# Kernel optimization log

Hardware: AMD Instinct MI355X
Metric: run time of the kernel (lower is better)

The kernel has to match this reference:

```python
import jax, jax.numpy as jnp
import numpy as np
from jax import lax

DIM = 384
NUM_HEADS = 6
STRIDE_Q = 1
STRIDE_KV = 2
BN_EPS = 1e-5
SCALE = DIM ** (-0.5)  # CvT scales by dim_out, not head_dim


def setup_inputs() -> dict:
    key = jax.random.key(0)
    ks = jax.random.split(key, 8)
    B, H, W, C = 32, 28, 28, DIM
    T = 1 + H * W
    x = jax.random.normal(ks[0], (B, T, C), dtype=jnp.float32)
    conv_w = jax.random.normal(ks[1], (3, C, 1, 3, 3), dtype=jnp.float32) * 0.1
    bn_gamma = jnp.ones((3, C), dtype=jnp.float32)
    bn_beta = jnp.zeros((3, C), dtype=jnp.float32)
    bn_mean = jnp.zeros((3, C), dtype=jnp.float32)
    bn_var = jnp.ones((3, C), dtype=jnp.float32)
    w_q = jax.random.normal(ks[2], (C, C), dtype=jnp.float32) * 0.02
    w_k = jax.random.normal(ks[3], (C, C), dtype=jnp.float32) * 0.02
    w_v = jax.random.normal(ks[4], (C, C), dtype=jnp.float32) * 0.02
    w_proj = jax.random.normal(ks[5], (C, C), dtype=jnp.float32) * 0.02
    b_proj = jnp.zeros((C,), dtype=jnp.float32)
    return {"x": x, "conv_w": conv_w, "bn_gamma": bn_gamma, "bn_beta": bn_beta,
            "bn_mean": bn_mean, "bn_var": bn_var, "w_q": w_q, "w_k": w_k,
            "w_v": w_v, "w_proj": w_proj, "b_proj": b_proj, "h": H, "w": W}


def _dw_conv_bn(x_sp, cw, gamma, beta, mean, var, stride):
    # x_sp: [B, C, H, W]; cw: [C, 1, 3, 3] depthwise (groups=C); inference BN
    C = x_sp.shape[1]
    y = lax.conv_general_dilated(
        x_sp, cw, window_strides=(stride, stride), padding=((1, 1), (1, 1)),
        feature_group_count=C, dimension_numbers=("NCHW", "OIHW", "NCHW"))
    inv = gamma * lax.rsqrt(var + BN_EPS)
    y = y * inv[None, :, None, None] + (beta - mean * inv)[None, :, None, None]
    B, Cc, Hc, Wc = y.shape
    return y.reshape(B, Cc, Hc * Wc).transpose(0, 2, 1)  # b (h w) c


def reference(x, conv_w, bn_gamma, bn_beta, bn_mean, bn_var,
              w_q, w_k, w_v, w_proj, b_proj, h, w):
    B, T, C = x.shape
    nh, hd = NUM_HEADS, C // NUM_HEADS
    cls_tok, x_tok = x[:, :1], x[:, 1:]
    x_sp = x_tok.reshape(B, h, w, C).transpose(0, 3, 1, 2)  # b c h w

    q = _dw_conv_bn(x_sp, conv_w[0], bn_gamma[0], bn_beta[0], bn_mean[0], bn_var[0], STRIDE_Q)
    k = _dw_conv_bn(x_sp, conv_w[1], bn_gamma[1], bn_beta[1], bn_mean[1], bn_var[1], STRIDE_KV)
    v = _dw_conv_bn(x_sp, conv_w[2], bn_gamma[2], bn_beta[2], bn_mean[2], bn_var[2], STRIDE_KV)

    q = jnp.concatenate([cls_tok, q], axis=1)
    k = jnp.concatenate([cls_tok, k], axis=1)
    v = jnp.concatenate([cls_tok, v], axis=1)

    def split_heads(t, wm):  # linear proj then b t (h d) -> b h t d
        t = t @ wm.T
        Bt, Tt, _ = t.shape
        return t.reshape(Bt, Tt, nh, hd).transpose(0, 2, 1, 3)

    q = split_heads(q, w_q)
    k = split_heads(k, w_k)
    v = split_heads(v, w_v)

    attn = jax.nn.softmax(jnp.einsum("bhld,bhtd->bhlt", q, k) * SCALE, axis=-1)
    out = jnp.einsum("bhlt,bhtd->bhld", attn, v)
    out = out.transpose(0, 2, 1, 3).reshape(B, -1, C)  # b t (h d)
    return out @ w_proj.T + b_proj
```

## Files before the change

kernel.cpp:

```cpp
#include <hip/hip_runtime.h>
#include <math.h>

#define B_SZ   32
#define C_DIM  384
#define H_IN   28
#define W_IN   28
#define TQ     785
#define TKV    197
#define NH     6
#define HD     64
#define SCALE_F 0.05103103630798287f
#define SCALE_L2E (0.05103103630798287f * 1.4426950408889634f)
#define BN_EPS_F 1e-5f

#define QROWS    25120
#define KVROWS   6304
#define QROWS_P  25344
#define KVROWS_P 6528
#define WELEM    147456
#define VT_LD    208

#define QT256    99
#define KVT256   25

typedef _Float16 f16;
typedef f16  f16x8 __attribute__((ext_vector_type(8)));
typedef f16  f16x4 __attribute__((ext_vector_type(4)));
typedef float f32x4 __attribute__((ext_vector_type(4)));

__device__ __forceinline__ void split16(float v, f16& h, f16& l) {
    h = (f16)v;
    l = (f16)(v - (float)h);
}

__device__ __forceinline__ void cp16(void* lds, const void* g) {
    __builtin_amdgcn_global_load_lds(
        (const __attribute__((address_space(1))) unsigned int*)g,
        (__attribute__((address_space(3))) unsigned int*)lds, 16, 0, 0);
}

__device__ __forceinline__ bool swz(int id, int yMax, int& y, int& n0) {
    int g = id / 24, w = id - g * 24;
    y = g * 8 + (w & 7);
    n0 = (w >> 3) * 128;
    return y < yMax;
}

__global__ __launch_bounds__(256) void prep_kernel(
    const float* __restrict__ wq, const float* __restrict__ wk,
    const float* __restrict__ wv, const float* __restrict__ wp,
    const float* __restrict__ conv_w,
    const float* __restrict__ gamma, const float* __restrict__ beta,
    const float* __restrict__ mean, const float* __restrict__ var,
    f16* __restrict__ Wh, f16* __restrict__ Wl,
    float* __restrict__ wAll)
{
    int idx = blockIdx.x * 256 + threadIdx.x;
    if (idx < 4 * WELEM) {
        int which = idx / WELEM, rem = idx - which * WELEM;
        const float* s = (which == 0) ? wq : (which == 1) ? wk : (which == 2) ? wv : wp;
        float v = s[rem];
        if (which == 0) v *= SCALE_L2E;
        f16 h, l;
        split16(v, h, l);
        Wh[idx] = h; Wl[idx] = l;
    } else if (idx < 4 * WELEM + 3 * C_DIM) {
        int k = idx - 4 * WELEM;
        int cv = k / C_DIM, c = k - cv * C_DIM;
        float inv = gamma[k] * rsqrtf(var[k] + BN_EPS_F);
#pragma unroll
        for (int t = 0; t < 9; ++t)
            wAll[cv * 3840 + t * C_DIM + c] = conv_w[(size_t)cv * C_DIM * 9 + c * 9 + t] * inv;
        wAll[cv * 3840 + 9 * C_DIM + c] = beta[k] - mean[k] * inv;
    }
}

__global__ __launch_bounds__(256) void fused_conv_kernel(
    const float* __restrict__ x,
    const float* __restrict__ wAll,
    f16* __restrict__ qh, f16* __restrict__ ql,
    f16* __restrict__ kh, f16* __restrict__ kl,
    f16* __restrict__ vh, f16* __restrict__ vl)
{
    __shared__ float sW[3 * 3840];
    int tid = threadIdx.x;
    int oi = blockIdx.x, b = blockIdx.y;

    if (oi == H_IN) {
        if (tid < 96) {
            int c = tid * 4;
            float4 v = *(const float4*)&x[(size_t)b * TQ * C_DIM + c];
            float a[4] = {v.x, v.y, v.z, v.w};
            f16x4 hv, lv;
#pragma unroll
            for (int u = 0; u < 4; ++u) { f16 h, l; split16(a[u], h, l); hv[u] = h; lv[u] = l; }
            size_t oq = (size_t)b * TQ * C_DIM + c;
            size_t okv = (size_t)b * TKV * C_DIM + c;
            *(f16x4*)&qh[oq] = hv;  *(f16x4*)&ql[oq] = lv;
            *(f16x4*)&kh[okv] = hv; *(f16x4*)&kl[okv] = lv;
            *(f16x4*)&vh[okv] = hv; *(f16x4*)&vl[okv] = lv;
        }
        return;
    }

#pragma unroll
    for (int i = 0; i < 12; ++i) {
        int idx = tid + 256 * i;
        if (idx < 2880) cp16(&sW[idx * 4], &wAll[idx * 4]);
    }
    __syncthreads();

    const size_t xb = (size_t)b * TQ * C_DIM + C_DIM;
    bool oi_even = (oi & 1) == 0;

    for (int it = 0; it < 11; ++it) {
        int idx = tid + 256 * it;
        if (idx >= 28 * 96) break;
        int oj = idx / 96, cg = idx - oj * 96;
        int c = cg * 4;

        float4 xv[9];
#pragma unroll
        for (int di = 0; di < 3; ++di) {
            int ii = oi + di - 1;
            bool rok = (ii >= 0) && (ii < H_IN);
#pragma unroll
            for (int dj = 0; dj < 3; ++dj) {
                int jj = oj + dj - 1;
                bool ok = rok && (jj >= 0) && (jj < W_IN);
                xv[di * 3 + dj] = ok ? *(const float4*)&x[xb + ((size_t)ii * W_IN + jj) * C_DIM + c]
                                     : make_float4(0.f, 0.f, 0.f, 0.f);
            }
        }

        {
            float4 acc = *(const float4*)&sW[0 * 3840 + 9 * C_DIM + c];
#pragma unroll
            for (int t = 0; t < 9; ++t) {
                float4 w4 = *(const float4*)&sW[0 * 3840 + t * C_DIM + c];
                acc.x += w4.x * xv[t].x; acc.y += w4.y * xv[t].y;
                acc.z += w4.z * xv[t].z; acc.w += w4.w * xv[t].w;
            }
            f16x4 hv, lv;
            float a[4] = {acc.x, acc.y, acc.z, acc.w};
#pragma unroll
            for (int u = 0; u < 4; ++u) { f16 h, l; split16(a[u], h, l); hv[u] = h; lv[u] = l; }
            size_t off = ((size_t)b * TQ + 1 + oi * W_IN + oj) * C_DIM + c;
            *(f16x4*)&qh[off] = hv;
            *(f16x4*)&ql[off] = lv;
        }

        if (oi_even && ((oj & 1) == 0)) {
            int p = (oi >> 1) * 14 + (oj >> 1);
            size_t off = ((size_t)b * TKV + 1 + p) * C_DIM + c;
#pragma unroll
            for (int cv = 1; cv <= 2; ++cv) {
                float4 acc = *(const float4*)&sW[cv * 3840 + 9 * C_DIM + c];
#pragma unroll
                for (int t = 0; t < 9; ++t) {
                    float4 w4 = *(const float4*)&sW[cv * 3840 + t * C_DIM + c];
                    acc.x += w4.x * xv[t].x; acc.y += w4.y * xv[t].y;
                    acc.z += w4.z * xv[t].z; acc.w += w4.w * xv[t].w;
                }
                f16x4 hv, lv;
                float a[4] = {acc.x, acc.y, acc.z, acc.w};
#pragma unroll
                for (int u = 0; u < 4; ++u) { f16 h, l; split16(a[u], h, l); hv[u] = h; lv[u] = l; }
                if (cv == 1) { *(f16x4*)&kh[off] = hv; *(f16x4*)&kl[off] = lv; }
                else         { *(f16x4*)&vh[off] = hv; *(f16x4*)&vl[off] = lv; }
            }
        }
    }
}

__device__ __forceinline__ void gemm_body(
    const f16* __restrict__ Ah, const f16* __restrict__ Al,
    const f16* __restrict__ Wh, const f16* __restrict__ Wl,
    const float* __restrict__ bias,
    float* __restrict__ Cf, f16* __restrict__ Coh, f16* __restrict__ Col,
    int M, int mode, int m0, int n0)
{
    __shared__ f16 lds[3 * 24576];

    const int t = threadIdx.x;
    const int wv = t >> 6, lane = t & 63;
    const int wr = (wv >> 1) * 64;
    const int wc = (wv & 1) * 64;
    const int lrow = lane & 15, quad = lane >> 4;
    const int qsw = quad ^ ((lrow >> 1) & 3);

    const int sr = t >> 2;
    const int g  = (t & 3) ^ ((t >> 3) & 3);

    const f16* gA0h = Ah + (size_t)(m0 + sr) * 384 + g * 8;
    const f16* gA1h = gA0h + 128 * 384;
    const f16* gA0l = Al + (size_t)(m0 + sr) * 384 + g * 8;
    const f16* gA1l = gA0l + 128 * 384;
    const f16* gBh  = Wh + (size_t)(n0 + sr) * 384 + g * 8;
    const f16* gBl  = Wl + (size_t)(n0 + sr) * 384 + g * 8;

#define STAGE(buf, kk) do {                                   \
        f16* d = lds + (buf) * 24576 + t * 8;                 \
        const int ko = (kk) * 32;                             \
        cp16(d,         gA0h + ko);                           \
        cp16(d + 4096,  gA1h + ko);                           \
        cp16(d + 8192,  gA0l + ko);                           \
        cp16(d + 12288, gA1l + ko);                           \
        cp16(d + 16384, gBh + ko);                            \
        cp16(d + 20480, gBl + ko);                            \
    } while (0)

    f32x4 acc[4][4];
#pragma unroll
    for (int i = 0; i < 4; ++i)
#pragma unroll
        for (int j = 0; j < 4; ++j)
            acc[i][j] = (f32x4){0.f, 0.f, 0.f, 0.f};

    STAGE(0, 0);
    STAGE(1, 1);

#pragma unroll
    for (int kk = 0; kk < 12; ++kk) {
        if (kk == 11) asm volatile("s_waitcnt vmcnt(0)" ::: "memory");
        else          asm volatile("s_waitcnt vmcnt(6)" ::: "memory");
        __builtin_amdgcn_s_barrier();
        __builtin_amdgcn_sched_barrier(0);

        if (kk < 10) {
            STAGE((kk + 2) % 3, kk + 2);
            __builtin_amdgcn_sched_barrier(0);
        }

        const f16* bp = lds + (kk % 3) * 24576;
        f16x8 ah[4], al[4], bh[4], bl[4];
#pragma unroll
        for (int i = 0; i < 4; ++i) {
            int ro = (wr + i * 16 + lrow) * 32 + qsw * 8;
            ah[i] = *(const f16x8*)&bp[ro];
            al[i] = *(const f16x8*)&bp[8192 + ro];
        }
#pragma unroll
        for (int j = 0; j < 4; ++j) {
            int ro = (wc + j * 16 + lrow) * 32 + qsw * 8;
            bh[j] = *(const f16x8*)&bp[16384 + ro];
            bl[j] = *(const f16x8*)&bp[20480 + ro];
        }
        asm volatile("s_waitcnt lgkmcnt(0)" ::: "memory");
        __builtin_amdgcn_sched_barrier(0);

        __builtin_amdgcn_s_setprio(1);
#pragma unroll
        for (int i = 0; i < 4; ++i)
#pragma unroll
            for (int j = 0; j < 4; ++j) {
                acc[i][j] = __builtin_amdgcn_mfma_f32_16x16x32_f16(ah[i], bh[j], acc[i][j], 0, 0, 0);
                acc[i][j] = __builtin_amdgcn_mfma_f32_16x16x32_f16(ah[i], bl[j], acc[i][j], 0, 0, 0);
                acc[i][j] = __builtin_amdgcn_mfma_f32_16x16x32_f16(al[i], bh[j], acc[i][j], 0, 0, 0);
            }
        __builtin_amdgcn_s_setprio(0);
    }
#undef STAGE

#pragma unroll
    for (int i = 0; i < 4; ++i) {
        int grow0 = m0 + wr + i * 16 + quad * 4;
#pragma unroll
        for (int j = 0; j < 4; ++j) {
            int gcol = n0 + wc + j * 16 + lrow;
            float bb = (bias && mode == 0) ? bias[gcol] : 0.f;
#pragma unroll
            for (int r = 0; r < 4; ++r) {
                int grow = grow0 + r;
                if (grow >= M) continue;
                float v = acc[i][j][r] + bb;
                if (mode == 0) {
                    Cf[(size_t)grow * 384 + gcol] = v;
                } else if (mode == 1) {
                    f16 h, l;
                    split16(v, h, l);
                    Coh[(size_t)grow * 384 + gcol] = h;
                    Col[(size_t)grow * 384 + gcol] = l;
                } else {
                    int bb2 = grow / TKV;
                    int key = grow - bb2 * TKV;
                    size_t off = (size_t)bb2 * 384 * VT_LD + (size_t)gcol * VT_LD + key;
                    Coh[off] = (f16)v;
                }
            }
        }
    }
}

__device__ __forceinline__ void gemm_body_s(
    const f16* __restrict__ Ah,
    const f16* __restrict__ Wh, const f16* __restrict__ Wl,
    const float* __restrict__ bias, float* __restrict__ Cf,
    int M, int m0, int n0)
{
    __shared__ f16 lds[3 * 16384];

    const int t = threadIdx.x;
    const int wv = t >> 6, lane = t & 63;
    const int wr = (wv >> 1) * 64;
    const int wc = (wv & 1) * 64;
    const int lrow = lane & 15, quad = lane >> 4;
    const int qsw = quad ^ ((lrow >> 1) & 3);

    const int sr = t >> 2;
    const int g  = (t & 3) ^ ((t >> 3) & 3);

    const f16* gA0 = Ah + (size_t)(m0 + sr) * 384 + g * 8;
    const f16* gA1 = gA0 + 128 * 384;
    const f16* gBh = Wh + (size_t)(n0 + sr) * 384 + g * 8;
    const f16* gBl = Wl + (size_t)(n0 + sr) * 384 + g * 8;

#define STAGE_S(buf, kk) do {                                 \
        f16* d = lds + (buf) * 16384 + t * 8;                 \
        const int ko = (kk) * 32;                             \
        cp16(d,         gA0 + ko);                            \
        cp16(d + 4096,  gA1 + ko);                            \
        cp16(d + 8192,  gBh + ko);                            \
        cp16(d + 12288, gBl + ko);                            \
    } while (0)

    f32x4 acc[4][4];
#pragma unroll
    for (int i = 0; i < 4; ++i)
#pragma unroll
        for (int j = 0; j < 4; ++j)
            acc[i][j] = (f32x4){0.f, 0.f, 0.f, 0.f};

    STAGE_S(0, 0);
    STAGE_S(1, 1);

#pragma unroll
    for (int kk = 0; kk < 12; ++kk) {
        if (kk == 11) asm volatile("s_waitcnt vmcnt(0)" ::: "memory");
        else          asm volatile("s_waitcnt vmcnt(4)" ::: "memory");
        __builtin_amdgcn_s_barrier();
        __builtin_amdgcn_sched_barrier(0);

        if (kk < 10) {
            STAGE_S((kk + 2) % 3, kk + 2);
            __builtin_amdgcn_sched_barrier(0);
        }

        const f16* bp = lds + (kk % 3) * 16384;
        f16x8 ah[4], bh[4], bl[4];
#pragma unroll
        for (int i = 0; i < 4; ++i) {
            int ro = (wr + i * 16 + lrow) * 32 + qsw * 8;
            ah[i] = *(const f16x8*)&bp[ro];
        }
#pragma unroll
        for (int j = 0; j < 4; ++j) {
            int ro = (wc + j * 16 + lrow) * 32 + qsw * 8;
            bh[j] = *(const f16x8*)&bp[8192 + ro];
            bl[j] = *(const f16x8*)&bp[12288 + ro];
        }
        asm volatile("s_waitcnt lgkmcnt(0)" ::: "memory");
        __builtin_amdgcn_sched_barrier(0);

        __builtin_amdgcn_s_setprio(1);
#pragma unroll
        for (int i = 0; i < 4; ++i)
#pragma unroll
            for (int j = 0; j < 4; ++j) {
                acc[i][j] = __builtin_amdgcn_mfma_f32_16x16x32_f16(ah[i], bh[j], acc[i][j], 0, 0, 0);
                acc[i][j] = __builtin_amdgcn_mfma_f32_16x16x32_f16(ah[i], bl[j], acc[i][j], 0, 0, 0);
            }
        __builtin_amdgcn_s_setprio(0);
    }
#undef STAGE_S

#pragma unroll
    for (int i = 0; i < 4; ++i) {
        int grow0 = m0 + wr + i * 16 + quad * 4;
#pragma unroll
        for (int j = 0; j < 4; ++j) {
            int gcol = n0 + wc + j * 16 + lrow;
            float bb = bias[gcol];
#pragma unroll
            for (int r = 0; r < 4; ++r) {
                int grow = grow0 + r;
                if (grow >= M) continue;
                Cf[(size_t)grow * 384 + gcol] = acc[i][j][r] + bb;
            }
        }
    }
}

__global__ __launch_bounds__(512, 2) void qkv_proj_kernel(
    const f16* __restrict__ qh, const f16* __restrict__ ql,
    const f16* __restrict__ kh, const f16* __restrict__ kl,
    const f16* __restrict__ vh, const f16* __restrict__ vl,
    const f16* __restrict__ Wh, const f16* __restrict__ Wl,
    f16* __restrict__ Qph, f16* __restrict__ Qpl,
    f16* __restrict__ Kph, f16* __restrict__ Kpl,
    f16* __restrict__ VTh,
    int yMax)
{
    int y, n0;
    if (!swz(blockIdx.x, yMax, y, n0)) return;
    if (y < QT256)
        gemm_body(qh, ql, Wh, Wl, nullptr, nullptr, Qph, Qpl, QROWS, 1, y * 256, n0);
    else if (y < QT256 + KVT256)
        gemm_body(kh, kl, Wh + WELEM, Wl + WELEM, nullptr, nullptr, Kph, Kpl,
                  KVROWS, 1, (y - QT256) * 256, n0);
    else
        gemm_body(vh, vl, Wh + 2 * WELEM, Wl + 2 * WELEM, nullptr, nullptr, VTh, nullptr,
                  KVROWS, 2, (y - QT256 - KVT256) * 256, n0);
}

__global__ __launch_bounds__(512, 2) void v_proj_kernel(
    const f16* __restrict__ vh, const f16* __restrict__ vl,
    const f16* __restrict__ Wh, const f16* __restrict__ Wl,
    f16* __restrict__ VTh)
{
    int y, n0;
    if (!swz(blockIdx.x, KVT256, y, n0)) return;
    gemm_body(vh, vl, Wh, Wl, nullptr, nullptr, VTh, nullptr, KVROWS, 2, y * 256, n0);
}

__global__ __launch_bounds__(512, 2) void out_proj_kernel(
    const f16* __restrict__ Ah,
    const f16* __restrict__ Wh, const f16* __restrict__ Wl,
    const float* __restrict__ bias, float* __restrict__ Cf)
{
    int y, n0;
    if (!swz(blockIdx.x, QT256, y, n0)) return;
    gemm_body_s(Ah, Wh, Wl, bias, Cf, QROWS, y * 256, n0);
}

__global__ __launch_bounds__(256) void attn_mfma6(
    const f16* __restrict__ Qh, const f16* __restrict__ Ql,
    const f16* __restrict__ Kh, const f16* __restrict__ Kl,
    const f16* __restrict__ VTh,
    f16* __restrict__ Oh)
{
    __shared__ f16 sQh[2][64][32];
    __shared__ f16 sQl[2][64][32];
    __shared__ f16 sKh[2][64][32];
    __shared__ f16 sKl[2][64][32];
    __shared__ float sPs[64][68];

    int t = threadIdx.x;
    int wv = t >> 6, lane = t & 63;
    int c = lane & 15, quad = lane >> 4;
    int wq0 = wv * 16;
    int h = blockIdx.y, b = blockIdx.z;
    int q0 = blockIdx.x * 64;

    const size_t qbase  = (size_t)b * TQ * C_DIM + h * HD;
    const size_t kbase  = (size_t)b * TKV * C_DIM + h * HD;
    const size_t vtbase = (size_t)b * 384 * VT_LD + (size_t)h * HD * VT_LD;

#pragma unroll
    for (int i = 0; i < 2; ++i) {
        int idx = t + 256 * i;
        int ks = idx >> 8, row = (idx >> 2) & 63, sg = (idx & 3) * 8;
        cp16(&sQh[ks][row][sg], &Qh[qbase + (size_t)(q0 + row) * C_DIM + ks * 32 + sg]);
        cp16(&sQl[ks][row][sg], &Ql[qbase + (size_t)(q0 + row) * C_DIM + ks * 32 + sg]);
    }

    f32x4 s[4][4];
#pragma unroll
    for (int kt = 0; kt < 4; ++kt)
#pragma unroll
        for (int j = 0; j < 4; ++j)
            s[kt][j] = (f32x4){0.f, 0.f, 0.f, 0.f};

#pragma unroll
    for (int kt = 0; kt < 4; ++kt) {
        if (kt) __syncthreads();
#pragma unroll
        for (int i = 0; i < 2; ++i) {
            int idx = t + 256 * i;
            int ks = idx >> 8, row = (idx >> 2) & 63, sg = (idx & 3) * 8;
            cp16(&sKh[ks][row][sg], &Kh[kbase + (size_t)(kt * 64 + row) * C_DIM + ks * 32 + sg]);
            cp16(&sKl[ks][row][sg], &Kl[kbase + (size_t)(kt * 64 + row) * C_DIM + ks * 32 + sg]);
        }
        __syncthreads();

#pragma unroll
        for (int ks = 0; ks < 2; ++ks) {
            f16x8 qh8 = *(const f16x8*)&sQh[ks][wq0 + c][quad * 8];
            f16x8 ql8 = *(const f16x8*)&sQl[ks][wq0 + c][quad * 8];
#pragma unroll
            for (int j = 0; j < 4; ++j) {
                f16x8 kh8 = *(const f16x8*)&sKh[ks][j * 16 + c][quad * 8];
                f16x8 kl8 = *(const f16x8*)&sKl[ks][j * 16 + c][quad * 8];
                s[kt][j] = __builtin_amdgcn_mfma_f32_16x16x32_f16(qh8, kh8, s[kt][j], 0, 0, 0);
                s[kt][j] = __builtin_amdgcn_mfma_f32_16x16x32_f16(qh8, kl8, s[kt][j], 0, 0, 0);
                s[kt][j] = __builtin_amdgcn_mfma_f32_16x16x32_f16(ql8, kh8, s[kt][j], 0, 0, 0);
            }
        }
    }

    __syncthreads();

#pragma unroll
    for (int i = 0; i < 2; ++i) {
        int idx = t + 256 * i;
        int ks = idx >> 8, row = (idx >> 2) & 63, sg = (idx & 3) * 8;
        cp16(&sKh[ks][row][sg], &VTh[vtbase + (size_t)row * VT_LD + ks * 32 + sg]);
        cp16(&sKl[ks][row][sg], &VTh[vtbase + (size_t)row * VT_LD + 64 + ks * 32 + sg]);
    }

#pragma unroll
    for (int r = 0; r < 4; ++r) {
        s[3][0][r] = (c < 5) ? s[3][0][r] : -1e30f;
        s[3][1][r] = -1e30f;
        s[3][2][r] = -1e30f;
        s[3][3][r] = -1e30f;
    }

    float inv_r[4];
#pragma unroll
    for (int r = 0; r < 4; ++r) {
        float mx = -1e30f;
#pragma unroll
        for (int kt = 0; kt < 4; ++kt)
#pragma unroll
            for (int j = 0; j < 4; ++j)
                mx = fmaxf(mx, s[kt][j][r]);
        mx = fmaxf(mx, __shfl_xor(mx, 1));
        mx = fmaxf(mx, __shfl_xor(mx, 2));
        mx = fmaxf(mx, __shfl_xor(mx, 4));
        mx = fmaxf(mx, __shfl_xor(mx, 8));
        float sum = 0.f;
#pragma unroll
        for (int kt = 0; kt < 4; ++kt)
#pragma unroll
            for (int j = 0; j < 4; ++j) {
                float pv = exp2f(s[kt][j][r] - mx);
                s[kt][j][r] = pv;
                sum += pv;
            }
        sum += __shfl_xor(sum, 1);
        sum += __shfl_xor(sum, 2);
        sum += __shfl_xor(sum, 4);
        sum += __shfl_xor(sum, 8);
        inv_r[r] = 1.f / sum;
    }

    f32x4 o[4];
#pragma unroll
    for (int j = 0; j < 4; ++j) o[j] = (f32x4){0.f, 0.f, 0.f, 0.f};

#define SPS_WRITE(VT) do {                                           \
        _Pragma("unroll") for (int r = 0; r < 4; ++r)                \
            _Pragma("unroll") for (int j = 0; j < 4; ++j)            \
                sPs[wq0 + quad * 4 + r][j * 16 + c] = s[VT][j][r];   \
    } while (0)

#define VT_ISSUE2(DST, VT) do {                                                \
        _Pragma("unroll") for (int i = 0; i < 2; ++i) {                        \
            int idx = t + 256 * i;                                             \
            int ks = idx >> 8, row = (idx >> 2) & 63, sg = (idx & 3) * 8;      \
            cp16(&DST[ks][row][sg],                                            \
                 &VTh[vtbase + (size_t)row * VT_LD + (VT) * 64 + ks * 32 + sg]); \
        } } while (0)

#define PV_TILE_S(BUF) do {                                                    \
        _Pragma("unroll") for (int ks = 0; ks < 2; ++ks) {                     \
            float4 p0 = *(const float4*)&sPs[wq0 + c][ks * 32 + quad * 8];     \
            float4 p1 = *(const float4*)&sPs[wq0 + c][ks * 32 + quad * 8 + 4]; \
            float pf[8] = {p0.x, p0.y, p0.z, p0.w, p1.x, p1.y, p1.z, p1.w};    \
            f16x8 p8;                                                          \
            _Pragma("unroll") for (int ii = 0; ii < 8; ++ii) p8[ii] = (f16)pf[ii]; \
            _Pragma("unroll") for (int j = 0; j < 4; ++j) {                    \
                f16x8 vv8 = *(const f16x8*)&BUF[ks][j * 16 + c][quad * 8];     \
                o[j] = __builtin_amdgcn_mfma_f32_16x16x32_f16(p8, vv8, o[j], 0, 0, 0); \
            } } } while (0)

    __syncthreads();
    SPS_WRITE(0);
    PV_TILE_S(sKh);
    __syncthreads();
    VT_ISSUE2(sKh, 2);
    SPS_WRITE(1);
    PV_TILE_S(sKl);
    __syncthreads();
    VT_ISSUE2(sKl, 3);
    SPS_WRITE(2);
    PV_TILE_S(sKh);
    __syncthreads();
    SPS_WRITE(3);
    PV_TILE_S(sKl);

#pragma unroll
    for (int r = 0; r < 4; ++r) {
        int gq = q0 + wq0 + quad * 4 + r;
        if (gq >= TQ) continue;
        float inv = inv_r[r];
#pragma unroll
        for (int j = 0; j < 4; ++j) {
            size_t off = (size_t)(b * TQ + gq) * C_DIM + h * HD + j * 16 + c;
            Oh[off] = (f16)(o[j][r] * inv);
        }
    }
#undef SPS_WRITE
#undef VT_ISSUE2
#undef PV_TILE_S
}

extern "C" void kernel_launch(void* const* d_in, const int* in_sizes, int n_in,
                              void* d_out, int out_size, void* d_ws, size_t ws_size,
                              hipStream_t stream) {
    const float* x       = (const float*)d_in[0];
    const float* conv_w  = (const float*)d_in[1];
    const float* bn_g    = (const float*)d_in[2];
    const float* bn_b    = (const float*)d_in[3];
    const float* bn_m    = (const float*)d_in[4];
    const float* bn_v    = (const float*)d_in[5];
    const float* w_q     = (const float*)d_in[6];
    const float* w_k     = (const float*)d_in[7];
    const float* w_v     = (const float*)d_in[8];
    const float* w_proj  = (const float*)d_in[9];
    const float* b_proj  = (const float*)d_in[10];
    float* out = (float*)d_out;

    const size_t QSZ   = (size_t)QROWS_P * 384 * sizeof(f16);
    const size_t KVSZ  = (size_t)KVROWS_P * 384 * sizeof(f16);
    const size_t WSZ   = 4 * (size_t)WELEM * sizeof(f16);
    const size_t VTSZ  = (size_t)B_SZ * 384 * VT_LD * sizeof(f16);
    const size_t WALLS = 3 * 3840 * sizeof(float);

    char* p = (char*)d_ws;
    f16* qh  = (f16*)p; p += QSZ;
    f16* ql  = (f16*)p; p += QSZ;
    f16* vh  = (f16*)p; p += KVSZ;
    f16* vl  = (f16*)p; p += KVSZ;
    f16* kh  = (f16*)p; p += KVSZ;
    f16* kl  = (f16*)p; p += KVSZ;
    f16* Wh  = (f16*)p; p += WSZ;
    f16* Wl  = (f16*)p; p += WSZ;
    f16* Qph = (f16*)p; p += QSZ;
    f16* Qpl = (f16*)p; p += QSZ;
    f16* Kph = (f16*)p; p += KVSZ;
    f16* Kpl = (f16*)p; p += KVSZ;
    float* wAll = (float*)p; p += WALLS;

    size_t used = (size_t)(p - (char*)d_ws);
    bool sepVT = (ws_size >= used + VTSZ);
    f16* VTh = sepVT ? (f16*)p : kh;
    f16* oh = qh;

    {
        int total = 4 * WELEM + 3 * C_DIM;
        prep_kernel<<<(total + 255) / 256, 256, 0, stream>>>(
            w_q, w_k, w_v, w_proj, conv_w, bn_g, bn_b, bn_m, bn_v, Wh, Wl, wAll);
    }

    {
        dim3 gc(H_IN + 1, B_SZ);
        fused_conv_kernel<<<gc, 256, 0, stream>>>(x, wAll, qh, ql, kh, kl, vh, vl);
    }

    if (sepVT) {
        int yMax = QT256 + 2 * KVT256;
        int nb = ((yMax + 7) / 8) * 24;
        qkv_proj_kernel<<<nb, 512, 0, stream>>>(qh, ql, kh, kl, vh, vl, Wh, Wl,
                                                Qph, Qpl, Kph, Kpl, VTh, yMax);
    } else {
        int yMax = QT256 + KVT256;
        int nb = ((yMax + 7) / 8) * 24;
        qkv_proj_kernel<<<nb, 512, 0, stream>>>(qh, ql, kh, kl, vh, vl, Wh, Wl,
                                                Qph, Qpl, Kph, Kpl, VTh, yMax);
        int nbv = ((KVT256 + 7) / 8) * 24;
        v_proj_kernel<<<nbv, 512, 0, stream>>>(vh, vl, Wh + 2 * WELEM, Wl + 2 * WELEM,
                                               VTh);
    }

    {
        dim3 ga((TQ + 63) / 64, NH, B_SZ);
        attn_mfma6<<<ga, 256, 0, stream>>>(Qph, Qpl, Kph, Kpl, VTh, oh);
    }

    {
        int nb = ((QT256 + 7) / 8) * 24;
        out_proj_kernel<<<nb, 512, 0, stream>>>(oh, Wh + 3 * WELEM, Wl + 3 * WELEM,
                                                b_proj, out);
    }
}
```

Before: 271.6 us.

## Drop hi/lo fp16 split for activations, use single fp16 Q/K/V paths

Conv outputs and the projected Q/K are now stored as a single fp16 tensor instead of a hi/lo split pair. The QKV projection reuses the 2-MFMA single-activation GEMM body, and attention QK^T uses one MFMA per tile instead of three. The new attention kernel also double-buffers the K tiles in shared memory. This roughly halves activation memory traffic and cuts MFMA work, at the cost of fp16 rounding of activations, which lowers accuracy relative to the fp32 reference.

Measured after the change: 243.3 us. 1.12x faster.

```diff
diff --git a/kernel.cpp b/kernel.cpp
--- a/kernel.cpp
+++ b/kernel.cpp
@@ -78,9 +78,7 @@
 __global__ __launch_bounds__(256) void fused_conv_kernel(
     const float* __restrict__ x,
     const float* __restrict__ wAll,
-    f16* __restrict__ qh, f16* __restrict__ ql,
-    f16* __restrict__ kh, f16* __restrict__ kl,
-    f16* __restrict__ vh, f16* __restrict__ vl)
+    f16* __restrict__ q, f16* __restrict__ k, f16* __restrict__ v)
 {
     __shared__ float sW[3 * 3840];
     int tid = threadIdx.x;
@@ -89,16 +87,16 @@
     if (oi == H_IN) {
         if (tid < 96) {
             int c = tid * 4;
-            float4 v = *(const float4*)&x[(size_t)b * TQ * C_DIM + c];
-            float a[4] = {v.x, v.y, v.z, v.w};
-            f16x4 hv, lv;
-#pragma unroll
-            for (int u = 0; u < 4; ++u) { f16 h, l; split16(a[u], h, l); hv[u] = h; lv[u] = l; }
+            float4 vv = *(const float4*)&x[(size_t)b * TQ * C_DIM + c];
+            float a[4] = {vv.x, vv.y, vv.z, vv.w};
+            f16x4 hv;
+#pragma unroll
+            for (int u = 0; u < 4; ++u) hv[u] = (f16)a[u];
             size_t oq = (size_t)b * TQ * C_DIM + c;
             size_t okv = (size_t)b * TKV * C_DIM + c;
-            *(f16x4*)&qh[oq] = hv;  *(f16x4*)&ql[oq] = lv;
-            *(f16x4*)&kh[okv] = hv; *(f16x4*)&kl[okv] = lv;
-            *(f16x4*)&vh[okv] = hv; *(f16x4*)&vl[okv] = lv;
+            *(f16x4*)&q[oq] = hv;
+            *(f16x4*)&k[okv] = hv;
+            *(f16x4*)&v[okv] = hv;
         }
         return;
     }
@@ -141,13 +139,10 @@
                 acc.x += w4.x * xv[t].x; acc.y += w4.y * xv[t].y;
                 acc.z += w4.z * xv[t].z; acc.w += w4.w * xv[t].w;
             }
-            f16x4 hv, lv;
-            float a[4] = {acc.x, acc.y, acc.z, acc.w};
-#pragma unroll
-            for (int u = 0; u < 4; ++u) { f16 h, l; split16(a[u], h, l); hv[u] = h; lv[u] = l; }
+            f16x4 hv;
+            hv[0] = (f16)acc.x; hv[1] = (f16)acc.y; hv[2] = (f16)acc.z; hv[3] = (f16)acc.w;
             size_t off = ((size_t)b * TQ + 1 + oi * W_IN + oj) * C_DIM + c;
-            *(f16x4*)&qh[off] = hv;
-            *(f16x4*)&ql[off] = lv;
+            *(f16x4*)&q[off] = hv;
         }
 
         if (oi_even && ((oj & 1) == 0)) {
@@ -162,131 +157,10 @@
                     acc.x += w4.x * xv[t].x; acc.y += w4.y * xv[t].y;
                     acc.z += w4.z * xv[t].z; acc.w += w4.w * xv[t].w;
                 }
-                f16x4 hv, lv;
-                float a[4] = {acc.x, acc.y, acc.z, acc.w};
-#pragma unroll
-                for (int u = 0; u < 4; ++u) { f16 h, l; split16(a[u], h, l); hv[u] = h; lv[u] = l; }
-                if (cv == 1) { *(f16x4*)&kh[off] = hv; *(f16x4*)&kl[off] = lv; }
-                else         { *(f16x4*)&vh[off] = hv; *(f16x4*)&vl[off] = lv; }
-            }
-        }
-    }
-}
-
-__device__ __forceinline__ void gemm_body(
-    const f16* __restrict__ Ah, const f16* __restrict__ Al,
-    const f16* __restrict__ Wh, const f16* __restrict__ Wl,
-    const float* __restrict__ bias,
-    float* __restrict__ Cf, f16* __restrict__ Coh, f16* __restrict__ Col,
-    int M, int mode, int m0, int n0)
-{
-    __shared__ f16 lds[3 * 24576];
-
-    const int t = threadIdx.x;
-    const int wv = t >> 6, lane = t & 63;
-    const int wr = (wv >> 1) * 64;
-    const int wc = (wv & 1) * 64;
-    const int lrow = lane & 15, quad = lane >> 4;
-    const int qsw = quad ^ ((lrow >> 1) & 3);
-
-    const int sr = t >> 2;
-    const int g  = (t & 3) ^ ((t >> 3) & 3);
-
-    const f16* gA0h = Ah + (size_t)(m0 + sr) * 384 + g * 8;
-    const f16* gA1h = gA0h + 128 * 384;
-    const f16* gA0l = Al + (size_t)(m0 + sr) * 384 + g * 8;
-    const f16* gA1l = gA0l + 128 * 384;
-    const f16* gBh  = Wh + (size_t)(n0 + sr) * 384 + g * 8;
-    const f16* gBl  = Wl + (size_t)(n0 + sr) * 384 + g * 8;
-
-#define STAGE(buf, kk) do {                                   \
-        f16* d = lds + (buf) * 24576 + t * 8;                 \
-        const int ko = (kk) * 32;                             \
-        cp16(d,         gA0h + ko);                           \
-        cp16(d + 4096,  gA1h + ko);                           \
-        cp16(d + 8192,  gA0l + ko);                           \
-        cp16(d + 12288, gA1l + ko);                           \
-        cp16(d + 16384, gBh + ko);                            \
-        cp16(d + 20480, gBl + ko);                            \
-    } while (0)
-
-    f32x4 acc[4][4];
-#pragma unroll
-    for (int i = 0; i < 4; ++i)
-#pragma unroll
-        for (int j = 0; j < 4; ++j)
-            acc[i][j] = (f32x4){0.f, 0.f, 0.f, 0.f};
-
-    STAGE(0, 0);
-    STAGE(1, 1);
-
-#pragma unroll
-    for (int kk = 0; kk < 12; ++kk) {
-        if (kk == 11) asm volatile("s_waitcnt vmcnt(0)" ::: "memory");
-        else          asm volatile("s_waitcnt vmcnt(6)" ::: "memory");
-        __builtin_amdgcn_s_barrier();
-        __builtin_amdgcn_sched_barrier(0);
-
-        if (kk < 10) {
-            STAGE((kk + 2) % 3, kk + 2);
-            __builtin_amdgcn_sched_barrier(0);
-        }
-
-        const f16* bp = lds + (kk % 3) * 24576;
-        f16x8 ah[4], al[4], bh[4], bl[4];
-#pragma unroll
-        for (int i = 0; i < 4; ++i) {
-            int ro = (wr + i * 16 + lrow) * 32 + qsw * 8;
-            ah[i] = *(const f16x8*)&bp[ro];
-            al[i] = *(const f16x8*)&bp[8192 + ro];
-        }
-#pragma unroll
-        for (int j = 0; j < 4; ++j) {
-            int ro = (wc + j * 16 + lrow) * 32 + qsw * 8;
-            bh[j] = *(const f16x8*)&bp[16384 + ro];
-            bl[j] = *(const f16x8*)&bp[20480 + ro];
-        }
-        asm volatile("s_waitcnt lgkmcnt(0)" ::: "memory");
-        __builtin_amdgcn_sched_barrier(0);
-
-        __builtin_amdgcn_s_setprio(1);
-#pragma unroll
-        for (int i = 0; i < 4; ++i)
-#pragma unroll
-            for (int j = 0; j < 4; ++j) {
-                acc[i][j] = __builtin_amdgcn_mfma_f32_16x16x32_f16(ah[i], bh[j], acc[i][j], 0, 0, 0);
-                acc[i][j] = __builtin_amdgcn_mfma_f32_16x16x32_f16(ah[i], bl[j], acc[i][j], 0, 0, 0);
-                acc[i][j] = __builtin_amdgcn_mfma_f32_16x16x32_f16(al[i], bh[j], acc[i][j], 0, 0, 0);
-            }
-        __builtin_amdgcn_s_setprio(0);
-    }
-#undef STAGE
-
-#pragma unroll
-    for (int i = 0; i < 4; ++i) {
-        int grow0 = m0 + wr + i * 16 + quad * 4;
-#pragma unroll
-        for (int j = 0; j < 4; ++j) {
-            int gcol = n0 + wc + j * 16 + lrow;
-            float bb = (bias && mode == 0) ? bias[gcol] : 0.f;
-#pragma unroll
-            for (int r = 0; r < 4; ++r) {
-                int grow = grow0 + r;
-                if (grow >= M) continue;
-                float v = acc[i][j][r] + bb;
-                if (mode == 0) {
-                    Cf[(size_t)grow * 384 + gcol] = v;
-                } else if (mode == 1) {
-                    f16 h, l;
-                    split16(v, h, l);
-                    Coh[(size_t)grow * 384 + gcol] = h;
-                    Col[(size_t)grow * 384 + gcol] = l;
-                } else {
-                    int bb2 = grow / TKV;
-                    int key = grow - bb2 * TKV;
-                    size_t off = (size_t)bb2 * 384 * VT_LD + (size_t)gcol * VT_LD + key;
-                    Coh[off] = (f16)v;
-                }
+                f16x4 hv;
+                hv[0] = (f16)acc.x; hv[1] = (f16)acc.y; hv[2] = (f16)acc.z; hv[3] = (f16)acc.w;
+                if (cv == 1) *(f16x4*)&k[off] = hv;
+                else         *(f16x4*)&v[off] = hv;
             }
         }
     }
@@ -295,8 +169,9 @@
 __device__ __forceinline__ void gemm_body_s(
     const f16* __restrict__ Ah,
     const f16* __restrict__ Wh, const f16* __restrict__ Wl,
-    const float* __restrict__ bias, float* __restrict__ Cf,
-    int M, int m0, int n0)
+    const float* __restrict__ bias,
+    float* __restrict__ Cf, f16* __restrict__ Co,
+    int M, int mode, int m0, int n0)
 {
     __shared__ f16 lds[3 * 16384];
 
@@ -380,47 +255,53 @@
 #pragma unroll
         for (int j = 0; j < 4; ++j) {
             int gcol = n0 + wc + j * 16 + lrow;
-            float bb = bias[gcol];
+            float bb = (bias && mode == 0) ? bias[gcol] : 0.f;
 #pragma unroll
             for (int r = 0; r < 4; ++r) {
                 int grow = grow0 + r;
                 if (grow >= M) continue;
-                Cf[(size_t)grow * 384 + gcol] = acc[i][j][r] + bb;
+                float vv = acc[i][j][r] + bb;
+                if (mode == 0) {
+                    Cf[(size_t)grow * 384 + gcol] = vv;
+                } else if (mode == 1) {
+                    Co[(size_t)grow * 384 + gcol] = (f16)vv;
+                } else {
+                    int bb2 = grow / TKV;
+                    int key = grow - bb2 * TKV;
+                    size_t off = (size_t)bb2 * 384 * VT_LD + (size_t)gcol * VT_LD + key;
+                    Co[off] = (f16)vv;
+                }
             }
         }
     }
 }
 
 __global__ __launch_bounds__(512, 2) void qkv_proj_kernel(
-    const f16* __restrict__ qh, const f16* __restrict__ ql,
-    const f16* __restrict__ kh, const f16* __restrict__ kl,
-    const f16* __restrict__ vh, const f16* __restrict__ vl,
+    const f16* __restrict__ q, const f16* __restrict__ k, const f16* __restrict__ v,
     const f16* __restrict__ Wh, const f16* __restrict__ Wl,
-    f16* __restrict__ Qph, f16* __restrict__ Qpl,
-    f16* __restrict__ Kph, f16* __restrict__ Kpl,
-    f16* __restrict__ VTh,
+    f16* __restrict__ Qp, f16* __restrict__ Kp, f16* __restrict__ VT,
     int yMax)
 {
     int y, n0;
     if (!swz(blockIdx.x, yMax, y, n0)) return;
     if (y < QT256)
-        gemm_body(qh, ql, Wh, Wl, nullptr, nullptr, Qph, Qpl, QROWS, 1, y * 256, n0);
+        gemm_body_s(q, Wh, Wl, nullptr, nullptr, Qp, QROWS, 1, y * 256, n0);
     else if (y < QT256 + KVT256)
-        gemm_body(kh, kl, Wh + WELEM, Wl + WELEM, nullptr, nullptr, Kph, Kpl,
-                  KVROWS, 1, (y - QT256) * 256, n0);
+        gemm_body_s(k, Wh + WELEM, Wl + WELEM, nullptr, nullptr, Kp,
+                    KVROWS, 1, (y - QT256) * 256, n0);
     else
-        gemm_body(vh, vl, Wh + 2 * WELEM, Wl + 2 * WELEM, nullptr, nullptr, VTh, nullptr,
-                  KVROWS, 2, (y - QT256 - KVT256) * 256, n0);
+        gemm_body_s(v, Wh + 2 * WELEM, Wl + 2 * WELEM, nullptr, nullptr, VT,
+                    KVROWS, 2, (y - QT256 - KVT256) * 256, n0);
 }
 
 __global__ __launch_bounds__(512, 2) void v_proj_kernel(
-    const f16* __restrict__ vh, const f16* __restrict__ vl,
+    const f16* __restrict__ v,
     const f16* __restrict__ Wh, const f16* __restrict__ Wl,
-    f16* __restrict__ VTh)
+    f16* __restrict__ VT)
 {
     int y, n0;
     if (!swz(blockIdx.x, KVT256, y, n0)) return;
-    gemm_body(vh, vl, Wh, Wl, nullptr, nullptr, VTh, nullptr, KVROWS, 2, y * 256, n0);
+    gemm_body_s(v, Wh, Wl, nullptr, nullptr, VT, KVROWS, 2, y * 256, n0);
 }
 
 __global__ __launch_bounds__(512, 2) void out_proj_kernel(
@@ -430,19 +311,16 @@
 {
     int y, n0;
     if (!swz(blockIdx.x, QT256, y, n0)) return;
-    gemm_body_s(Ah, Wh, Wl, bias, Cf, QROWS, y * 256, n0);
-}
-
-__global__ __launch_bounds__(256) void attn_mfma6(
-    const f16* __restrict__ Qh, const f16* __restrict__ Ql,
-    const f16* __restrict__ Kh, const f16* __restrict__ Kl,
-    const f16* __restrict__ VTh,
-    f16* __restrict__ Oh)
-{
-    __shared__ f16 sQh[2][64][32];
-    __shared__ f16 sQl[2][64][32];
-    __shared__ f16 sKh[2][64][32];
-    __shared__ f16 sKl[2][64][32];
+    gemm_body_s(Ah, Wh, Wl, bias, Cf, nullptr, QROWS, 0, y * 256, n0);
+}
+
+__global__ __launch_bounds__(256) void attn_mfma7(
+    const f16* __restrict__ Qp, const f16* __restrict__ Kp,
+    const f16* __restrict__ VT, f16* __restrict__ Oh)
+{
+    __shared__ f16 sQ[2][64][32];
+    __shared__ f16 sKa[2][64][32];
+    __shared__ f16 sKb[2][64][32];
     __shared__ float sPs[64][68];
 
     int t = threadIdx.x;
@@ -456,13 +334,22 @@
     const size_t kbase  = (size_t)b * TKV * C_DIM + h * HD;
     const size_t vtbase = (size_t)b * 384 * VT_LD + (size_t)h * HD * VT_LD;
 
-#pragma unroll
-    for (int i = 0; i < 2; ++i) {
-        int idx = t + 256 * i;
-        int ks = idx >> 8, row = (idx >> 2) & 63, sg = (idx & 3) * 8;
-        cp16(&sQh[ks][row][sg], &Qh[qbase + (size_t)(q0 + row) * C_DIM + ks * 32 + sg]);
-        cp16(&sQl[ks][row][sg], &Ql[qbase + (size_t)(q0 + row) * C_DIM + ks * 32 + sg]);
-    }
+#define STAGE_T(DST, EXPR) do {                                      \
+        _Pragma("unroll") for (int i = 0; i < 2; ++i) {              \
+            int idx = t + 256 * i;                                   \
+            int ks = idx >> 8, row = (idx >> 2) & 63, sg = (idx & 3) * 8; \
+            cp16(&DST[ks][row][sg], (EXPR));                         \
+        } } while (0)
+
+#define QK(KT, BUF) do {                                             \
+        __builtin_amdgcn_s_setprio(1);                               \
+        _Pragma("unroll") for (int ks = 0; ks < 2; ++ks) {           \
+            _Pragma("unroll") for (int j = 0; j < 4; ++j) {          \
+                f16x8 k8 = *(const f16x8*)&BUF[ks][j * 16 + c][quad * 8]; \
+                s[KT][j] = __builtin_amdgcn_mfma_f32_16x16x32_f16(q8[ks], k8, s[KT][j], 0, 0, 0); \
+            } }                                                      \
+        __builtin_amdgcn_s_setprio(0);                               \
+    } while (0)
 
     f32x4 s[4][4];
 #pragma unroll
@@ -471,42 +358,29 @@
         for (int j = 0; j < 4; ++j)
             s[kt][j] = (f32x4){0.f, 0.f, 0.f, 0.f};
 
-#pragma unroll
-    for (int kt = 0; kt < 4; ++kt) {
-        if (kt) __syncthreads();
-#pragma unroll
-        for (int i = 0; i < 2; ++i) {
-            int idx = t + 256 * i;
-            int ks = idx >> 8, row = (idx >> 2) & 63, sg = (idx & 3) * 8;
-            cp16(&sKh[ks][row][sg], &Kh[kbase + (size_t)(kt * 64 + row) * C_DIM + ks * 32 + sg]);
-            cp16(&sKl[ks][row][sg], &Kl[kbase + (size_t)(kt * 64 + row) * C_DIM + ks * 32 + sg]);
-        }
-        __syncthreads();
-
-#pragma unroll
-        for (int ks = 0; ks < 2; ++ks) {
-            f16x8 qh8 = *(const f16x8*)&sQh[ks][wq0 + c][quad * 8];
-            f16x8 ql8 = *(const f16x8*)&sQl[ks][wq0 + c][quad * 8];
-#pragma unroll
-            for (int j = 0; j < 4; ++j) {
-                f16x8 kh8 = *(const f16x8*)&sKh[ks][j * 16 + c][quad * 8];
-                f16x8 kl8 = *(const f16x8*)&sKl[ks][j * 16 + c][quad * 8];
-                s[kt][j] = __builtin_amdgcn_mfma_f32_16x16x32_f16(qh8, kh8, s[kt][j], 0, 0, 0);
-                s[kt][j] = __builtin_amdgcn_mfma_f32_16x16x32_f16(qh8, kl8, s[kt][j], 0, 0, 0);
-                s[kt][j] = __builtin_amdgcn_mfma_f32_16x16x32_f16(ql8, kh8, s[kt][j], 0, 0, 0);
-            }
-        }
-    }
-
-    __syncthreads();
-
-#pragma unroll
-    for (int i = 0; i < 2; ++i) {
-        int idx = t + 256 * i;
-        int ks = idx >> 8, row = (idx >> 2) & 63, sg = (idx & 3) * 8;
-        cp16(&sKh[ks][row][sg], &VTh[vtbase + (size_t)row * VT_LD + ks * 32 + sg]);
-        cp16(&sKl[ks][row][sg], &VTh[vtbase + (size_t)row * VT_LD + 64 + ks * 32 + sg]);
-    }
+    STAGE_T(sQ,  &Qp[qbase + (size_t)(q0 + row) * C_DIM + ks * 32 + sg]);
+    STAGE_T(sKa, &Kp[kbase + (size_t)(0 * 64 + row) * C_DIM + ks * 32 + sg]);
+    __syncthreads();
+
+    f16x8 q8[2];
+#pragma unroll
+    for (int ks = 0; ks < 2; ++ks)
+        q8[ks] = *(const f16x8*)&sQ[ks][wq0 + c][quad * 8];
+
+    STAGE_T(sKb, &Kp[kbase + (size_t)(1 * 64 + row) * C_DIM + ks * 32 + sg]);
+    QK(0, sKa);
+    __syncthreads();
+    STAGE_T(sKa, &Kp[kbase + (size_t)(2 * 64 + row) * C_DIM + ks * 32 + sg]);
+    QK(1, sKb);
+    __syncthreads();
+    STAGE_T(sKb, &Kp[kbase + (size_t)(3 * 64 + row) * C_DIM + ks * 32 + sg]);
+    QK(2, sKa);
+    __syncthreads();
+    QK(3, sKb);
+    __syncthreads();
+
+    STAGE_T(sKa, &VT[vtbase + (size_t)row * VT_LD + 0 * 64 + ks * 32 + sg]);
+    STAGE_T(sKb, &VT[vtbase + (size_t)row * VT_LD + 1 * 64 + ks * 32 + sg]);
 
 #pragma unroll
     for (int r = 0; r < 4; ++r) {
@@ -549,46 +423,41 @@
 #pragma unroll
     for (int j = 0; j < 4; ++j) o[j] = (f32x4){0.f, 0.f, 0.f, 0.f};
 
-#define SPS_WRITE(VT) do {                                           \
+#define SPS_WRITE(VTI) do {                                          \
         _Pragma("unroll") for (int r = 0; r < 4; ++r)                \
             _Pragma("unroll") for (int j = 0; j < 4; ++j)            \
-                sPs[wq0 + quad * 4 + r][j * 16 + c] = s[VT][j][r];   \
+                sPs[wq0 + quad * 4 + r][j * 16 + c] = s[VTI][j][r];  \
     } while (0)
 
-#define VT_ISSUE2(DST, VT) do {                                                \
-        _Pragma("unroll") for (int i = 0; i < 2; ++i) {                        \
-            int idx = t + 256 * i;                                             \
-            int ks = idx >> 8, row = (idx >> 2) & 63, sg = (idx & 3) * 8;      \
-            cp16(&DST[ks][row][sg],                                            \
-                 &VTh[vtbase + (size_t)row * VT_LD + (VT) * 64 + ks * 32 + sg]); \
+#define PV(BUF) do {                                                 \
+        _Pragma("unroll") for (int ks = 0; ks < 2; ++ks) {           \
+            float4 p0 = *(const float4*)&sPs[wq0 + c][ks * 32 + quad * 8]; \
+            float4 p1 = *(const float4*)&sPs[wq0 + c][ks * 32 + quad * 8 + 4]; \
+            f16x8 p8;                                                \
+            p8[0] = (f16)p0.x; p8[1] = (f16)p0.y; p8[2] = (f16)p0.z; p8[3] = (f16)p0.w; \
+            p8[4] = (f16)p1.x; p8[5] = (f16)p1.y; p8[6] = (f16)p1.z; p8[7] = (f16)p1.w; \
+            __builtin_amdgcn_s_setprio(1);                           \
+            _Pragma("unroll") for (int j = 0; j < 4; ++j) {          \
+                f16x8 v8 = *(const f16x8*)&BUF[ks][j * 16 + c][quad * 8]; \
+                o[j] = __builtin_amdgcn_mfma_f32_16x16x32_f16(p8, v8, o[j], 0, 0, 0); \
+            }                                                        \
+            __builtin_amdgcn_s_setprio(0);                           \
         } } while (0)
 
-#define PV_TILE_S(BUF) do {                                                    \
-        _Pragma("unroll") for (int ks = 0; ks < 2; ++ks) {                     \
-            float4 p0 = *(const float4*)&sPs[wq0 + c][ks * 32 + quad * 8];     \
-            float4 p1 = *(const float4*)&sPs[wq0 + c][ks * 32 + quad * 8 + 4]; \
-            float pf[8] = {p0.x, p0.y, p0.z, p0.w, p1.x, p1.y, p1.z, p1.w};    \
-            f16x8 p8;                                                          \
-            _Pragma("unroll") for (int ii = 0; ii < 8; ++ii) p8[ii] = (f16)pf[ii]; \
-            _Pragma("unroll") for (int j = 0; j < 4; ++j) {                    \
-                f16x8 vv8 = *(const f16x8*)&BUF[ks][j * 16 + c][quad * 8];     \
-                o[j] = __builtin_amdgcn_mfma_f32_16x16x32_f16(p8, vv8, o[j], 0, 0, 0); \
-            } } } while (0)
-
     __syncthreads();
     SPS_WRITE(0);
-    PV_TILE_S(sKh);
-    __syncthreads();
-    VT_ISSUE2(sKh, 2);
+    PV(sKa);
+    __syncthreads();
+    STAGE_T(sKa, &VT[vtbase + (size_t)row * VT_LD + 2 * 64 + ks * 32 + sg]);
     SPS_WRITE(1);
-    PV_TILE_S(sKl);
-    __syncthreads();
-    VT_ISSUE2(sKl, 3);
+    PV(sKb);
+    __syncthreads();
+    STAGE_T(sKb, &VT[vtbase + (size_t)row * VT_LD + 3 * 64 + ks * 32 + sg]);
     SPS_WRITE(2);
-    PV_TILE_S(sKh);
+    PV(sKa);
     __syncthreads();
     SPS_WRITE(3);
-    PV_TILE_S(sKl);
+    PV(sKb);
 
 #pragma unroll
     for (int r = 0; r < 4; ++r) {
@@ -601,9 +470,10 @@
             Oh[off] = (f16)(o[j][r] * inv);
         }
     }
+#undef STAGE_T
+#undef QK
 #undef SPS_WRITE
-#undef VT_ISSUE2
-#undef PV_TILE_S
+#undef PV
 }
 
 extern "C" void kernel_launch(void* const* d_in, const int* in_sizes, int n_in,
@@ -622,31 +492,26 @@
     const float* b_proj  = (const float*)d_in[10];
     float* out = (float*)d_out;
 
-    const size_t QSZ   = (size_t)QROWS_P * 384 * sizeof(f16);
-    const size_t KVSZ  = (size_t)KVROWS_P * 384 * sizeof(f16);
+    const size_t QS    = (size_t)QROWS_P * 384 * sizeof(f16);
+    const size_t KVS   = (size_t)KVROWS_P * 384 * sizeof(f16);
     const size_t WSZ   = 4 * (size_t)WELEM * sizeof(f16);
-    const size_t VTSZ  = (size_t)B_SZ * 384 * VT_LD * sizeof(f16);
+    const size_t VTS   = (size_t)B_SZ * 384 * VT_LD * sizeof(f16);
     const size_t WALLS = 3 * 3840 * sizeof(float);
 
     char* p = (char*)d_ws;
-    f16* qh  = (f16*)p; p += QSZ;
-    f16* ql  = (f16*)p; p += QSZ;
-    f16* vh  = (f16*)p; p += KVSZ;
-    f16* vl  = (f16*)p; p += KVSZ;
-    f16* kh  = (f16*)p; p += KVSZ;
-    f16* kl  = (f16*)p; p += KVSZ;
+    f16* q   = (f16*)p; p += QS;
+    f16* k   = (f16*)p; p += KVS;
+    f16* v   = (f16*)p; p += KVS;
     f16* Wh  = (f16*)p; p += WSZ;
     f16* Wl  = (f16*)p; p += WSZ;
-    f16* Qph = (f16*)p; p += QSZ;
-    f16* Qpl = (f16*)p; p += QSZ;
-    f16* Kph = (f16*)p; p += KVSZ;
-    f16* Kpl = (f16*)p; p += KVSZ;
+    f16* Qp  = (f16*)p; p += QS;
+    f16* Kp  = (f16*)p; p += KVS;
     float* wAll = (float*)p; p += WALLS;
 
     size_t used = (size_t)(p - (char*)d_ws);
-    bool sepVT = (ws_size >= used + VTSZ);
-    f16* VTh = sepVT ? (f16*)p : kh;
-    f16* oh = qh;
+    bool sepVT = (ws_size >= used + VTS);
+    f16* VT = sepVT ? (f16*)p : k;
+    f16* oh = q;
 
     {
         int total = 4 * WELEM + 3 * C_DIM;
@@ -656,27 +521,24 @@
 
     {
         dim3 gc(H_IN + 1, B_SZ);
-        fused_conv_kernel<<<gc, 256, 0, stream>>>(x, wAll, qh, ql, kh, kl, vh, vl);
+        fused_conv_kernel<<<gc, 256, 0, stream>>>(x, wAll, q, k, v);
     }
 
     if (sepVT) {
         int yMax = QT256 + 2 * KVT256;
         int nb = ((yMax + 7) / 8) * 24;
-        qkv_proj_kernel<<<nb, 512, 0, stream>>>(qh, ql, kh, kl, vh, vl, Wh, Wl,
-                                                Qph, Qpl, Kph, Kpl, VTh, yMax);
+        qkv_proj_kernel<<<nb, 512, 0, stream>>>(q, k, v, Wh, Wl, Qp, Kp, VT, yMax);
     } else {
         int yMax = QT256 + KVT256;
         int nb = ((yMax + 7) / 8) * 24;
-        qkv_proj_kernel<<<nb, 512, 0, stream>>>(qh, ql, kh, kl, vh, vl, Wh, Wl,
-                                                Qph, Qpl, Kph, Kpl, VTh, yMax);
+        qkv_proj_kernel<<<nb, 512, 0, stream>>>(q, k, v, Wh, Wl, Qp, Kp, VT, yMax);
         int nbv = ((KVT256 + 7) / 8) * 24;
-        v_proj_kernel<<<nbv, 512, 0, stream>>>(vh, vl, Wh + 2 * WELEM, Wl + 2 * WELEM,
-                                               VTh);
+        v_proj_kernel<<<nbv, 512, 0, stream>>>(v, Wh + 2 * WELEM, Wl + 2 * WELEM, VT);
     }
 
     {
         dim3 ga((TQ + 63) / 64, NH, B_SZ);
-        attn_mfma6<<<ga, 256, 0, stream>>>(Qph, Qpl, Kph, Kpl, VTh, oh);
+        attn_mfma7<<<ga, 256, 0, stream>>>(Qp, Kp, VT, oh);
     }
 
     {
```
